# Kernel optimization log

Measured on AMD Instinct MI355X. Metric: run time of the kernel, lower is better.

The kernel has to match this reference:

```python
import jax, jax.numpy as jnp
import numpy as np
from jax import lax

PATCH = 16
TAU = 0.5
EPS = 1e-8  # torch CosineSimilarity default eps


def setup_inputs() -> dict:
    key = jax.random.key(0)
    k1, k2, k3, k4, k5 = jax.random.split(key, 5)
    B, C, HW = 64, 3, 384
    hidden, latent = 768, 1024
    return {
        "x": jax.random.normal(k1, (B, C, HW, HW), dtype=jnp.float32),
        "conv_w": jax.random.normal(k2, (hidden, C, PATCH, PATCH), dtype=jnp.float32) * 0.02,
        "conv_b": jax.random.normal(k3, (hidden,), dtype=jnp.float32) * 0.02,
        "latent1": jax.random.normal(k4, (1, latent, hidden), dtype=jnp.float32),
        "latent2": jax.random.normal(k5, (1, latent, hidden), dtype=jnp.float32),
    }


def _cosine_scores(p, p_norm, lat):
    # p: (B, N, D); lat: (L, D) -> (B, N, L) cosine similarity
    l_norm = jnp.linalg.norm(lat, axis=-1)  # (L,)
    dots = jnp.einsum('bnd,ld->bnl', p, lat)
    denom = jnp.maximum(p_norm[:, :, None] * l_norm[None, None, :], EPS)
    return dots / denom


def reference(x, conv_w, conv_b, latent1, latent2):
    # Patch embedding: Conv2d(kernel=stride=16, padding=0)
    patch = lax.conv_general_dilated(
        x, conv_w, window_strides=(PATCH, PATCH), padding='VALID',
        dimension_numbers=('NCHW', 'OIHW', 'NCHW'))
    patch = patch + conv_b[None, :, None, None]  # (B, D, H', W')
    B, D = patch.shape[0], patch.shape[1]
    p = patch.reshape(B, D, -1).transpose(0, 2, 1)  # (B, N, D)
    p_norm = jnp.linalg.norm(p, axis=-1)  # (B, N)

    far = _cosine_scores(p, p_norm, latent1[0])    # (B, N, L)
    close = _cosine_scores(p, p_norm, latent2[0])  # (B, N, L)

    sum_close = jnp.sum(jnp.exp(close / TAU), axis=(1, 2))  # (B,)
    sum_far = jnp.sum(jnp.exp(far / TAU), axis=(1, 2))      # (B,)
    loss = -jnp.log(sum_close / sum_far)
    return loss.mean()
```

## Files before the change

kernel.cpp:

```cpp
#include <hip/hip_runtime.h>
#include <math.h>

using f32x4  = __attribute__((ext_vector_type(4))) float;
using bf16x8 = __attribute__((ext_vector_type(8))) short;

typedef const __attribute__((address_space(1))) void gas_void;
typedef __attribute__((address_space(3))) void las_void;

__device__ __forceinline__ void gl16(const void* g, void* l) {
    __builtin_amdgcn_global_load_lds((gas_void*)g, (las_void*)l, 16, 0, 0);
}

__device__ __forceinline__ unsigned short f2bf(float f) {
    union { float f; unsigned u; } v; v.f = f;
    unsigned r = v.u + 0x7fffu + ((v.u >> 16) & 1u);
    return (unsigned short)(r >> 16);
}
__device__ __forceinline__ float bf2f(unsigned short u) {
    return __uint_as_float(((unsigned)u) << 16);
}

#define VW0() asm volatile("s_waitcnt vmcnt(0)")
#define BAR() __builtin_amdgcn_s_barrier()

__global__ void pcl_prep_x(const float* __restrict__ x, unsigned short* __restrict__ xp) {
    int t = threadIdx.x;
    int wv = t >> 6, l = t & 63;
    int p = blockIdx.x * 4 + wv;
    int b = p / 576, n = p % 576;
    int ph = n / 24, pw = n % 24;
    const float* base = x + ((size_t)(b * 3)) * 147456 + (ph * 16) * 384 + pw * 16;
    unsigned* dst = (unsigned*)(xp + (size_t)p * 768);
#pragma unroll
    for (int q = 0; q < 6; ++q) {
        int k = q * 128 + l * 2;
        int c = k >> 8, i = (k >> 4) & 15, j = k & 15;
        const float* s = base + (size_t)c * 147456 + i * 384 + j;
        float2 v = *(const float2*)s;
        unsigned lo = f2bf(v.x), hi = f2bf(v.y);
        dst[q * 64 + l] = lo | (hi << 16);
    }
}

__global__ void pcl_prep_wl(const float* __restrict__ w,
                            const float* __restrict__ l1, const float* __restrict__ l2,
                            unsigned short* __restrict__ wsW,
                            unsigned short* __restrict__ wsL) {
    int r = blockIdx.x, t = threadIdx.x;
    if (r < 768) {
        const float* src = w + (size_t)r * 768;
        unsigned short* dst = wsW + (size_t)r * 768;
#pragma unroll
        for (int i = 0; i < 12; ++i) dst[t + 64 * i] = f2bf(src[t + 64 * i]);
    } else {
        int lr = r - 768;
        const float* src = (lr < 1024) ? l1 + (size_t)lr * 768 : l2 + (size_t)(lr - 1024) * 768;
        unsigned short* dst = wsL + (size_t)lr * 768;
        float vals[12];
        float s = 0.f;
#pragma unroll
        for (int i = 0; i < 12; ++i) {
            float f = bf2f(f2bf(src[t + 64 * i]));
            vals[i] = f; s += f * f;
        }
#pragma unroll
        for (int off = 32; off; off >>= 1) s += __shfl_xor(s, off, 64);
        float rn = 1.0f / sqrtf(s);
#pragma unroll
        for (int i = 0; i < 12; ++i) dst[t + 64 * i] = f2bf(vals[i] * rn);
    }
}

#define K1_LDS 81920

__global__ __launch_bounds__(256, 2)
void pcl_k1(const unsigned short* __restrict__ xp,
            const unsigned short* __restrict__ wsW,
            const float* __restrict__ bias,
            unsigned short* __restrict__ pbuf,
            float* __restrict__ rpnp) {
    extern __shared__ char smem[];
    const int t = threadIdx.x, w = t >> 6, l = t & 63;
    const int wg = (blockIdx.x & 7) * 192 + (blockIdx.x >> 3);
    const int mt = wg >> 3, nt = wg & 7;
    const size_t Mb = (size_t)mt * 192;
    const int Nb = nt * 96;
    const int wm = w >> 1, wn = w & 1;
    const int ir = l >> 3, s2 = (l & 7) ^ ir;
    const int lm = l & 15, lg4 = l >> 4;

    char* buf0 = smem;
    char* buf1 = smem + 40960;

    auto stage = [&](int kt, char* buf) {
#pragma unroll
        for (int rr = 0; rr < 6; ++rr) {
            int c2 = w * 6 + rr;
            gl16(xp + (Mb + c2 * 8 + ir) * 768 + kt * 64 + s2 * 8, buf + c2 * 1024);
        }
#pragma unroll
        for (int rr = 0; rr < 3; ++rr) {
            int c2 = w * 3 + rr;
            gl16(wsW + (size_t)(Nb + c2 * 8 + ir) * 768 + kt * 64 + s2 * 8,
                 buf + 24576 + c2 * 1024);
        }
    };

    f32x4 acc[6][3];
#pragma unroll
    for (int m = 0; m < 6; ++m)
#pragma unroll
        for (int nb = 0; nb < 3; ++nb) acc[m][nb] = (f32x4)0.f;

    stage(0, buf0);
    VW0(); BAR();

    bf16x8 areg[3][2], breg[3][2];

#pragma unroll 2
    for (int kt = 0; kt < 12; ++kt) {
        char* cur = (kt & 1) ? buf1 : buf0;
        char* nxt = (kt & 1) ? buf0 : buf1;

        if (kt < 11) stage(kt + 1, nxt);

#pragma unroll
        for (int nb = 0; nb < 3; ++nb)
#pragma unroll
            for (int ks = 0; ks < 2; ++ks) {
                int rb = wn * 48 + nb * 16 + lm, slot = ks * 4 + lg4;
                breg[nb][ks] = *(const bf16x8*)(cur + 24576 + rb * 128 + ((slot ^ (rb & 7)) << 4));
            }
#pragma unroll
        for (int m = 0; m < 3; ++m)
#pragma unroll
            for (int ks = 0; ks < 2; ++ks) {
                int r = wm * 96 + m * 16 + lm, slot = ks * 4 + lg4;
                areg[m][ks] = *(const bf16x8*)(cur + r * 128 + ((slot ^ (r & 7)) << 4));
            }
        __builtin_amdgcn_s_setprio(1);
#pragma unroll
        for (int m = 0; m < 3; ++m)
#pragma unroll
            for (int nb = 0; nb < 3; ++nb)
#pragma unroll
                for (int ks = 0; ks < 2; ++ks)
                    acc[m][nb] = __builtin_amdgcn_mfma_f32_16x16x32_bf16(areg[m][ks], breg[nb][ks], acc[m][nb], 0, 0, 0);
        __builtin_amdgcn_s_setprio(0);

#pragma unroll
        for (int m = 0; m < 3; ++m)
#pragma unroll
            for (int ks = 0; ks < 2; ++ks) {
                int r = wm * 96 + 48 + m * 16 + lm, slot = ks * 4 + lg4;
                areg[m][ks] = *(const bf16x8*)(cur + r * 128 + ((slot ^ (r & 7)) << 4));
            }
        __builtin_amdgcn_s_setprio(1);
#pragma unroll
        for (int m = 0; m < 3; ++m)
#pragma unroll
            for (int nb = 0; nb < 3; ++nb)
#pragma unroll
                for (int ks = 0; ks < 2; ++ks)
                    acc[3 + m][nb] = __builtin_amdgcn_mfma_f32_16x16x32_bf16(areg[m][ks], breg[nb][ks], acc[3 + m][nb], 0, 0, 0);
        __builtin_amdgcn_s_setprio(0);

        VW0();
        BAR();
    }

    float rs[6][4];
#pragma unroll
    for (int m = 0; m < 6; ++m)
#pragma unroll
        for (int j = 0; j < 4; ++j) rs[m][j] = 0.f;
#pragma unroll
    for (int nb = 0; nb < 3; ++nb) {
        int d = Nb + wn * 48 + nb * 16 + lm;
        float bv = bias[d];
#pragma unroll
        for (int m = 0; m < 6; ++m) {
            int mh = m / 3, mi = m % 3;
#pragma unroll
            for (int j = 0; j < 4; ++j) {
                int row = wm * 96 + mh * 48 + mi * 16 + lg4 * 4 + j;
                unsigned short h = f2bf(acc[m][nb][j] + bv);
                pbuf[(Mb + row) * 768 + d] = h;
                float fv = bf2f(h);
                rs[m][j] += fv * fv;
            }
        }
    }
#pragma unroll
    for (int m = 0; m < 6; ++m)
#pragma unroll
        for (int j = 0; j < 4; ++j) {
            rs[m][j] += __shfl_xor(rs[m][j], 1);
            rs[m][j] += __shfl_xor(rs[m][j], 2);
            rs[m][j] += __shfl_xor(rs[m][j], 4);
            rs[m][j] += __shfl_xor(rs[m][j], 8);
        }
    __syncthreads();
    float* nrm = (float*)smem;
    if (lm == 0) {
#pragma unroll
        for (int m = 0; m < 6; ++m) {
            int mh = m / 3, mi = m % 3;
#pragma unroll
            for (int j = 0; j < 4; ++j) {
                int row = wm * 96 + mh * 48 + mi * 16 + lg4 * 4 + j;
                nrm[row * 2 + wn] = rs[m][j];
            }
        }
    }
    __syncthreads();
    if (t < 192) rpnp[(size_t)nt * 36864 + Mb + t] = nrm[t * 2] + nrm[t * 2 + 1];
}

__global__ void pcl_norm(const float* __restrict__ rpnp, float* __restrict__ rpn) {
    int i = blockIdx.x * 256 + threadIdx.x;
    float s = 0.f;
#pragma unroll
    for (int nt = 0; nt < 8; ++nt) s += rpnp[(size_t)nt * 36864 + i];
    rpn[i] = 1.0f / sqrtf(s);
}

#define K2_LDS 81920

__global__ __launch_bounds__(256, 2)
void pcl_k2(const unsigned short* __restrict__ pbuf,
            const unsigned short* __restrict__ wsL,
            const float* __restrict__ rpn,
            double* __restrict__ partials) {
    extern __shared__ char smem[];
    const int t = threadIdx.x, w = t >> 6, l = t & 63;
    const int wg = (blockIdx.x & 7) * 384 + (blockIdx.x >> 3);
    const int mt = wg >> 4, nt = wg & 15;
    const size_t Mb = (size_t)mt * 192;
    const int Nb = nt * 128;
    const int wm = w >> 1, wn = w & 1;
    const int ir = l >> 3, s2 = (l & 7) ^ ir;
    const int lm = l & 15, lg4 = l >> 4;

    char* buf0 = smem;
    char* buf1 = smem + 40960;

    auto stage = [&](int kt, char* buf) {
#pragma unroll
        for (int rr = 0; rr < 6; ++rr) {
            int c2 = w * 6 + rr;
            gl16(pbuf + (Mb + c2 * 8 + ir) * 768 + kt * 64 + s2 * 8, buf + c2 * 1024);
        }
#pragma unroll
        for (int rr = 0; rr < 4; ++rr) {
            int c2 = w * 4 + rr;
            gl16(wsL + (size_t)(Nb + c2 * 8 + ir) * 768 + kt * 64 + s2 * 8,
                 buf + 24576 + c2 * 1024);
        }
    };

    f32x4 acc[6][4];
#pragma unroll
    for (int m = 0; m < 6; ++m)
#pragma unroll
        for (int nb = 0; nb < 4; ++nb) acc[m][nb] = (f32x4)0.f;

    stage(0, buf0);
    VW0(); BAR();

    bf16x8 areg[3][2], breg[4][2];

#pragma unroll 2
    for (int kt = 0; kt < 12; ++kt) {
        char* cur = (kt & 1) ? buf1 : buf0;
        char* nxt = (kt & 1) ? buf0 : buf1;

        if (kt < 11) stage(kt + 1, nxt);

#pragma unroll
        for (int nb = 0; nb < 4; ++nb)
#pragma unroll
            for (int ks = 0; ks < 2; ++ks) {
                int rb = wn * 64 + nb * 16 + lm, slot = ks * 4 + lg4;
                breg[nb][ks] = *(const bf16x8*)(cur + 24576 + rb * 128 + ((slot ^ (rb & 7)) << 4));
            }
#pragma unroll
        for (int m = 0; m < 3; ++m)
#pragma unroll
            for (int ks = 0; ks < 2; ++ks) {
                int r = wm * 96 + m * 16 + lm, slot = ks * 4 + lg4;
                areg[m][ks] = *(const bf16x8*)(cur + r * 128 + ((slot ^ (r & 7)) << 4));
            }
        __builtin_amdgcn_s_setprio(1);
#pragma unroll
        for (int m = 0; m < 3; ++m)
#pragma unroll
            for (int nb = 0; nb < 4; ++nb)
#pragma unroll
                for (int ks = 0; ks < 2; ++ks)
                    acc[m][nb] = __builtin_amdgcn_mfma_f32_16x16x32_bf16(areg[m][ks], breg[nb][ks], acc[m][nb], 0, 0, 0);
        __builtin_amdgcn_s_setprio(0);

#pragma unroll
        for (int m = 0; m < 3; ++m)
#pragma unroll
            for (int ks = 0; ks < 2; ++ks) {
                int r = wm * 96 + 48 + m * 16 + lm, slot = ks * 4 + lg4;
                areg[m][ks] = *(const bf16x8*)(cur + r * 128 + ((slot ^ (r & 7)) << 4));
            }
        __builtin_amdgcn_s_setprio(1);
#pragma unroll
        for (int m = 0; m < 3; ++m)
#pragma unroll
            for (int nb = 0; nb < 4; ++nb)
#pragma unroll
                for (int ks = 0; ks < 2; ++ks)
                    acc[3 + m][nb] = __builtin_amdgcn_mfma_f32_16x16x32_bf16(areg[m][ks], breg[nb][ks], acc[3 + m][nb], 0, 0, 0);
        __builtin_amdgcn_s_setprio(0);

        VW0();
        BAR();
    }

    double ssum = 0.0;
#pragma unroll
    for (int m = 0; m < 6; ++m) {
        int mh = m / 3, mi = m % 3;
        int rl = wm * 96 + mh * 48 + mi * 16;
        float rv[4];
#pragma unroll
        for (int j = 0; j < 4; ++j) rv[j] = rpn[Mb + rl + lg4 * 4 + j];
        float es = 0.f;
#pragma unroll
        for (int nb = 0; nb < 4; ++nb)
#pragma unroll
            for (int j = 0; j < 4; ++j)
                es += __expf(2.0f * acc[m][nb][j] * rv[j]);
        ssum += (double)es;
    }
#pragma unroll
    for (int off = 32; off; off >>= 1) ssum += __shfl_down(ssum, off);
    __syncthreads();
    double* red = (double*)smem;
    if (l == 0) red[w] = ssum;
    __syncthreads();
    if (t == 0) {
        double s = 0.0;
#pragma unroll
        for (int i = 0; i < 4; ++i) s += red[i];
        partials[wg] = s;
    }
}

__global__ void pcl_finish(const double* __restrict__ partials, float* __restrict__ out) {
    int b = threadIdx.x;
    double far = 0.0, close = 0.0;
#pragma unroll
    for (int i = 0; i < 3; ++i) {
        int mt = b * 3 + i;
#pragma unroll
        for (int nTile = 0; nTile < 16; ++nTile) {
            double v = partials[mt * 16 + nTile];
            if (nTile < 8) far += v; else close += v;
        }
    }
    double lb = log(far) - log(close);
#pragma unroll
    for (int off = 32; off; off >>= 1) lb += __shfl_down(lb, off);
    if (b == 0) out[0] = (float)(lb * (1.0 / 64.0));
}

extern "C" void kernel_launch(void* const* d_in, const int* in_sizes, int n_in,
                              void* d_out, int out_size, void* d_ws, size_t ws_size,
                              hipStream_t stream) {
    const float* x    = (const float*)d_in[0];
    const float* w    = (const float*)d_in[1];
    const float* bias = (const float*)d_in[2];
    const float* l1   = (const float*)d_in[3];
    const float* l2   = (const float*)d_in[4];
    float* out = (float*)d_out;

    unsigned short* xp   = (unsigned short*)d_ws;
    unsigned short* pbuf = (unsigned short*)((char*)d_ws + 56623104);
    unsigned short* wsW  = (unsigned short*)((char*)d_ws + 113246208);
    unsigned short* wsL  = (unsigned short*)((char*)d_ws + 114425856);
    float* rpnp          = (float*)((char*)d_ws + 117571584);
    float* rpn           = (float*)((char*)d_ws + 118751232);
    double* partials     = (double*)((char*)d_ws + 118898688);

    (void)hipFuncSetAttribute((const void*)pcl_k1,
                              hipFuncAttributeMaxDynamicSharedMemorySize, K1_LDS);
    (void)hipFuncSetAttribute((const void*)pcl_k2,
                              hipFuncAttributeMaxDynamicSharedMemorySize, K2_LDS);

    pcl_prep_x<<<9216, 256, 0, stream>>>(x, xp);
    pcl_prep_wl<<<2816, 64, 0, stream>>>(w, l1, l2, wsW, wsL);
    pcl_k1<<<1536, 256, K1_LDS, stream>>>(xp, wsW, bias, pbuf, rpnp);
    pcl_norm<<<144, 256, 0, stream>>>(rpnp, rpn);
    pcl_k2<<<3072, 256, K2_LDS, stream>>>(pbuf, wsL, rpn, partials);
    pcl_finish<<<1, 64, 0, stream>>>(partials, out);
}
```

Before: 194.8 us.

## Load A operand directly to registers, stage only B through LDS

In both GEMM kernels the A-tile (patch rows) is no longer staged through LDS. Each wave now loads its own A fragments from global memory straight into double-buffered registers, while only the B tile still goes through the LDS double buffer. The wait before each barrier becomes a partial vmcnt(12), so the next tile's A register loads can stay in flight across the barrier. A sched_barrier pins the order of the issued loads. This cuts LDS traffic and footprint, and it saves the separate LDS reads for A. The cost is much higher VGPR pressure from two 6x2 A register sets, A global loads that are not coalesced, and reliance on an exact vmcnt count.

```diff
diff --git a/kernel.cpp b/kernel.cpp
--- a/kernel.cpp
+++ b/kernel.cpp
@@ -20,8 +20,10 @@
     return __uint_as_float(((unsigned)u) << 16);
 }
 
-#define VW0() asm volatile("s_waitcnt vmcnt(0)")
+#define VWB() asm volatile("s_waitcnt vmcnt(12)" ::: "memory")
+#define VW0() asm volatile("s_waitcnt vmcnt(0)" ::: "memory")
 #define BAR() __builtin_amdgcn_s_barrier()
+#define SCHEDPIN() __builtin_amdgcn_sched_barrier(0)
 
 __global__ void pcl_prep_x(const float* __restrict__ x, unsigned short* __restrict__ xp) {
     int t = threadIdx.x;
@@ -71,7 +73,7 @@
     }
 }
 
-#define K1_LDS 81920
+#define K1_LDS 24576
 
 __global__ __launch_bounds__(256, 2)
 void pcl_k1(const unsigned short* __restrict__ xp,
@@ -90,20 +92,27 @@
     const int lm = l & 15, lg4 = l >> 4;
 
     char* buf0 = smem;
-    char* buf1 = smem + 40960;
-
-    auto stage = [&](int kt, char* buf) {
-#pragma unroll
-        for (int rr = 0; rr < 6; ++rr) {
-            int c2 = w * 6 + rr;
-            gl16(xp + (Mb + c2 * 8 + ir) * 768 + kt * 64 + s2 * 8, buf + c2 * 1024);
-        }
+    char* buf1 = smem + 12288;
+
+    const unsigned short* pA = xp + (Mb + wm * 96 + lm) * 768 + lg4 * 8;
+
+    auto stageB = [&](int kt, char* buf) {
 #pragma unroll
         for (int rr = 0; rr < 3; ++rr) {
             int c2 = w * 3 + rr;
             gl16(wsW + (size_t)(Nb + c2 * 8 + ir) * 768 + kt * 64 + s2 * 8,
-                 buf + 24576 + c2 * 1024);
-        }
+                 buf + c2 * 1024);
+        }
+    };
+    auto loadA = [&](int kt, bf16x8 (&aN)[6][2]) {
+#pragma unroll
+        for (int mh = 0; mh < 2; ++mh)
+#pragma unroll
+            for (int mi = 0; mi < 3; ++mi)
+#pragma unroll
+                for (int ks = 0; ks < 2; ++ks)
+                    aN[mh * 3 + mi][ks] = *(const bf16x8*)
+                        (pA + (size_t)(mh * 48 + mi * 16) * 768 + kt * 64 + ks * 32);
     };
 
     f32x4 acc[6][3];
@@ -112,61 +121,37 @@
 #pragma unroll
         for (int nb = 0; nb < 3; ++nb) acc[m][nb] = (f32x4)0.f;
 
-    stage(0, buf0);
+    bf16x8 aP[6][2], aQ[6][2], breg[3][2];
+
+    loadA(0, aP);
+    stageB(0, buf0);
     VW0(); BAR();
 
-    bf16x8 areg[3][2], breg[3][2];
-
-#pragma unroll 2
-    for (int kt = 0; kt < 12; ++kt) {
-        char* cur = (kt & 1) ? buf1 : buf0;
-        char* nxt = (kt & 1) ? buf0 : buf1;
-
-        if (kt < 11) stage(kt + 1, nxt);
-
+    auto body = [&](int kt, bf16x8 (&aC)[6][2], bf16x8 (&aN)[6][2], char* cur, char* nxt) {
+        if (kt < 11) { stageB(kt + 1, nxt); SCHEDPIN(); loadA(kt + 1, aN); }
 #pragma unroll
         for (int nb = 0; nb < 3; ++nb)
 #pragma unroll
             for (int ks = 0; ks < 2; ++ks) {
                 int rb = wn * 48 + nb * 16 + lm, slot = ks * 4 + lg4;
-                breg[nb][ks] = *(const bf16x8*)(cur + 24576 + rb * 128 + ((slot ^ (rb & 7)) << 4));
-            }
-#pragma unroll
-        for (int m = 0; m < 3; ++m)
-#pragma unroll
-            for (int ks = 0; ks < 2; ++ks) {
-                int r = wm * 96 + m * 16 + lm, slot = ks * 4 + lg4;
-                areg[m][ks] = *(const bf16x8*)(cur + r * 128 + ((slot ^ (r & 7)) << 4));
+                breg[nb][ks] = *(const bf16x8*)(cur + rb * 128 + ((slot ^ (rb & 7)) << 4));
             }
         __builtin_amdgcn_s_setprio(1);
 #pragma unroll
-        for (int m = 0; m < 3; ++m)
+        for (int m = 0; m < 6; ++m)
 #pragma unroll
             for (int nb = 0; nb < 3; ++nb)
 #pragma unroll
                 for (int ks = 0; ks < 2; ++ks)
-                    acc[m][nb] = __builtin_amdgcn_mfma_f32_16x16x32_bf16(areg[m][ks], breg[nb][ks], acc[m][nb], 0, 0, 0);
+                    acc[m][nb] = __builtin_amdgcn_mfma_f32_16x16x32_bf16(aC[m][ks], breg[nb][ks], acc[m][nb], 0, 0, 0);
         __builtin_amdgcn_s_setprio(0);
-
-#pragma unroll
-        for (int m = 0; m < 3; ++m)
-#pragma unroll
-            for (int ks = 0; ks < 2; ++ks) {
-                int r = wm * 96 + 48 + m * 16 + lm, slot = ks * 4 + lg4;
-                areg[m][ks] = *(const bf16x8*)(cur + r * 128 + ((slot ^ (r & 7)) << 4));
-            }
-        __builtin_amdgcn_s_setprio(1);
-#pragma unroll
-        for (int m = 0; m < 3; ++m)
-#pragma unroll
-            for (int nb = 0; nb < 3; ++nb)
-#pragma unroll
-                for (int ks = 0; ks < 2; ++ks)
-                    acc[3 + m][nb] = __builtin_amdgcn_mfma_f32_16x16x32_bf16(areg[m][ks], breg[nb][ks], acc[3 + m][nb], 0, 0, 0);
-        __builtin_amdgcn_s_setprio(0);
-
-        VW0();
+        if (kt < 11) { VWB(); } else { VW0(); }
         BAR();
+    };
+
+    for (int kp = 0; kp < 6; ++kp) {
+        body(2 * kp,     aP, aQ, buf0, buf1);
+        body(2 * kp + 1, aQ, aP, buf1, buf0);
     }
 
     float rs[6][4];
@@ -225,7 +210,7 @@
     rpn[i] = 1.0f / sqrtf(s);
 }
 
-#define K2_LDS 81920
+#define K2_LDS 32768
 
 __global__ __launch_bounds__(256, 2)
 void pcl_k2(const unsigned short* __restrict__ pbuf,
@@ -243,20 +228,27 @@
     const int lm = l & 15, lg4 = l >> 4;
 
     char* buf0 = smem;
-    char* buf1 = smem + 40960;
-
-    auto stage = [&](int kt, char* buf) {
-#pragma unroll
-        for (int rr = 0; rr < 6; ++rr) {
-            int c2 = w * 6 + rr;
-            gl16(pbuf + (Mb + c2 * 8 + ir) * 768 + kt * 64 + s2 * 8, buf + c2 * 1024);
-        }
+    char* buf1 = smem + 16384;
+
+    const unsigned short* pA = pbuf + (Mb + wm * 96 + lm) * 768 + lg4 * 8;
+
+    auto stageB = [&](int kt, char* buf) {
 #pragma unroll
         for (int rr = 0; rr < 4; ++rr) {
             int c2 = w * 4 + rr;
             gl16(wsL + (size_t)(Nb + c2 * 8 + ir) * 768 + kt * 64 + s2 * 8,
-                 buf + 24576 + c2 * 1024);
-        }
+                 buf + c2 * 1024);
+        }
+    };
+    auto loadA = [&](int kt, bf16x8 (&aN)[6][2]) {
+#pragma unroll
+        for (int mh = 0; mh < 2; ++mh)
+#pragma unroll
+            for (int mi = 0; mi < 3; ++mi)
+#pragma unroll
+                for (int ks = 0; ks < 2; ++ks)
+                    aN[mh * 3 + mi][ks] = *(const bf16x8*)
+                        (pA + (size_t)(mh * 48 + mi * 16) * 768 + kt * 64 + ks * 32);
     };
 
     f32x4 acc[6][4];
@@ -265,61 +257,37 @@
 #pragma unroll
         for (int nb = 0; nb < 4; ++nb) acc[m][nb] = (f32x4)0.f;
 
-    stage(0, buf0);
+    bf16x8 aP[6][2], aQ[6][2], breg[4][2];
+
+    loadA(0, aP);
+    stageB(0, buf0);
     VW0(); BAR();
 
-    bf16x8 areg[3][2], breg[4][2];
-
-#pragma unroll 2
-    for (int kt = 0; kt < 12; ++kt) {
-        char* cur = (kt & 1) ? buf1 : buf0;
-        char* nxt = (kt & 1) ? buf0 : buf1;
-
-        if (kt < 11) stage(kt + 1, nxt);
-
+    auto body = [&](int kt, bf16x8 (&aC)[6][2], bf16x8 (&aN)[6][2], char* cur, char* nxt) {
+        if (kt < 11) { stageB(kt + 1, nxt); SCHEDPIN(); loadA(kt + 1, aN); }
 #pragma unroll
         for (int nb = 0; nb < 4; ++nb)
 #pragma unroll
             for (int ks = 0; ks < 2; ++ks) {
                 int rb = wn * 64 + nb * 16 + lm, slot = ks * 4 + lg4;
-                breg[nb][ks] = *(const bf16x8*)(cur + 24576 + rb * 128 + ((slot ^ (rb & 7)) << 4));
-            }
-#pragma unroll
-        for (int m = 0; m < 3; ++m)
-#pragma unroll
-            for (int ks = 0; ks < 2; ++ks) {
-                int r = wm * 96 + m * 16 + lm, slot = ks * 4 + lg4;
-                areg[m][ks] = *(const bf16x8*)(cur + r * 128 + ((slot ^ (r & 7)) << 4));
+                breg[nb][ks] = *(const bf16x8*)(cur + rb * 128 + ((slot ^ (rb & 7)) << 4));
             }
         __builtin_amdgcn_s_setprio(1);
 #pragma unroll
-        for (int m = 0; m < 3; ++m)
+        for (int m = 0; m < 6; ++m)
 #pragma unroll
             for (int nb = 0; nb < 4; ++nb)
 #pragma unroll
                 for (int ks = 0; ks < 2; ++ks)
-                    acc[m][nb] = __builtin_amdgcn_mfma_f32_16x16x32_bf16(areg[m][ks], breg[nb][ks], acc[m][nb], 0, 0, 0);
+                    acc[m][nb] = __builtin_amdgcn_mfma_f32_16x16x32_bf16(aC[m][ks], breg[nb][ks], acc[m][nb], 0, 0, 0);
         __builtin_amdgcn_s_setprio(0);
-
-#pragma unroll
-        for (int m = 0; m < 3; ++m)
-#pragma unroll
-            for (int ks = 0; ks < 2; ++ks) {
-                int r = wm * 96 + 48 + m * 16 + lm, slot = ks * 4 + lg4;
-                areg[m][ks] = *(const bf16x8*)(cur + r * 128 + ((slot ^ (r & 7)) << 4));
-            }
-        __builtin_amdgcn_s_setprio(1);
-#pragma unroll
-        for (int m = 0; m < 3; ++m)
-#pragma unroll
-            for (int nb = 0; nb < 4; ++nb)
-#pragma unroll
-                for (int ks = 0; ks < 2; ++ks)
-                    acc[3 + m][nb] = __builtin_amdgcn_mfma_f32_16x16x32_bf16(areg[m][ks], breg[nb][ks], acc[3 + m][nb], 0, 0, 0);
-        __builtin_amdgcn_s_setprio(0);
-
-        VW0();
+        if (kt < 11) { VWB(); } else { VW0(); }
         BAR();
+    };
+
+    for (int kp = 0; kp < 6; ++kp) {
+        body(2 * kp,     aP, aQ, buf0, buf1);
+        body(2 * kp + 1, aQ, aP, buf1, buf0);
     }
 
     double ssum = 0.0;
```

New measurement: 406.0 us. 108% more time.

## Load GEMM A operand directly from global into registers, shrink LDS to B only

Applied to the files above, without the earlier changes.

The second GEMM kernel now uses 512 threads (8 waves) with each wave owning 48 rows, loading the patch-embedding A operand straight from global memory into registers instead of staging it through LDS. Only the latent B tile is double-buffered in LDS, shrinking shared memory from 80 KB to 32 KB so more blocks fit per CU. A partial vmcnt wait and sched_barrier pins keep the B prefetch in flight. The trade-off is uncoalesced per-lane 16-byte global loads for A with latency exposed in the loop, plus fewer accumulators per wave.

```diff
diff --git a/kernel.cpp b/kernel.cpp
--- a/kernel.cpp
+++ b/kernel.cpp
@@ -20,8 +20,10 @@
     return __uint_as_float(((unsigned)u) << 16);
 }
 
-#define VW0() asm volatile("s_waitcnt vmcnt(0)")
+#define VW2() asm volatile("s_waitcnt vmcnt(2)" ::: "memory")
+#define VW0() asm volatile("s_waitcnt vmcnt(0)" ::: "memory")
 #define BAR() __builtin_amdgcn_s_barrier()
+#define SCHEDPIN() __builtin_amdgcn_sched_barrier(0)
 
 __global__ void pcl_prep_x(const float* __restrict__ x, unsigned short* __restrict__ xp) {
     int t = threadIdx.x;
@@ -225,9 +227,9 @@
     rpn[i] = 1.0f / sqrtf(s);
 }
 
-#define K2_LDS 81920
-
-__global__ __launch_bounds__(256, 2)
+#define K2_LDS 32768
+
+__global__ __launch_bounds__(512, 4)
 void pcl_k2(const unsigned short* __restrict__ pbuf,
             const unsigned short* __restrict__ wsL,
             const float* __restrict__ rpn,
@@ -243,53 +245,51 @@
     const int lm = l & 15, lg4 = l >> 4;
 
     char* buf0 = smem;
-    char* buf1 = smem + 40960;
-
-    auto stage = [&](int kt, char* buf) {
-#pragma unroll
-        for (int rr = 0; rr < 6; ++rr) {
-            int c2 = w * 6 + rr;
-            gl16(pbuf + (Mb + c2 * 8 + ir) * 768 + kt * 64 + s2 * 8, buf + c2 * 1024);
-        }
-#pragma unroll
-        for (int rr = 0; rr < 4; ++rr) {
-            int c2 = w * 4 + rr;
+    char* buf1 = smem + 16384;
+
+    const unsigned short* pA = pbuf + (Mb + wm * 48 + lm) * 768 + lg4 * 8;
+
+    auto stageB = [&](int kt, char* buf) {
+#pragma unroll
+        for (int rr = 0; rr < 2; ++rr) {
+            int c2 = w * 2 + rr;
             gl16(wsL + (size_t)(Nb + c2 * 8 + ir) * 768 + kt * 64 + s2 * 8,
-                 buf + 24576 + c2 * 1024);
+                 buf + c2 * 1024);
         }
     };
 
-    f32x4 acc[6][4];
-#pragma unroll
-    for (int m = 0; m < 6; ++m)
+    f32x4 acc[3][4];
+#pragma unroll
+    for (int m = 0; m < 3; ++m)
 #pragma unroll
         for (int nb = 0; nb < 4; ++nb) acc[m][nb] = (f32x4)0.f;
 
-    stage(0, buf0);
-    VW0(); BAR();
-
-    bf16x8 areg[3][2], breg[4][2];
+    bf16x8 a[3][2], breg[4][2];
+
+    stageB(0, buf0);
 
 #pragma unroll 2
     for (int kt = 0; kt < 12; ++kt) {
         char* cur = (kt & 1) ? buf1 : buf0;
         char* nxt = (kt & 1) ? buf0 : buf1;
 
-        if (kt < 11) stage(kt + 1, nxt);
+        if (kt < 11) stageB(kt + 1, nxt);
+        SCHEDPIN();
+#pragma unroll
+        for (int mi = 0; mi < 3; ++mi)
+#pragma unroll
+            for (int ks = 0; ks < 2; ++ks)
+                a[mi][ks] = *(const bf16x8*)(pA + (size_t)(mi * 16) * 768 + kt * 64 + ks * 32);
+        SCHEDPIN();
+        if (kt < 11) { VW2(); } else { VW0(); }
+        BAR();
 
 #pragma unroll
         for (int nb = 0; nb < 4; ++nb)
 #pragma unroll
             for (int ks = 0; ks < 2; ++ks) {
                 int rb = wn * 64 + nb * 16 + lm, slot = ks * 4 + lg4;
-                breg[nb][ks] = *(const bf16x8*)(cur + 24576 + rb * 128 + ((slot ^ (rb & 7)) << 4));
-            }
-#pragma unroll
-        for (int m = 0; m < 3; ++m)
-#pragma unroll
-            for (int ks = 0; ks < 2; ++ks) {
-                int r = wm * 96 + m * 16 + lm, slot = ks * 4 + lg4;
-                areg[m][ks] = *(const bf16x8*)(cur + r * 128 + ((slot ^ (r & 7)) << 4));
+                breg[nb][ks] = *(const bf16x8*)(cur + rb * 128 + ((slot ^ (rb & 7)) << 4));
             }
         __builtin_amdgcn_s_setprio(1);
 #pragma unroll
@@ -298,35 +298,15 @@
             for (int nb = 0; nb < 4; ++nb)
 #pragma unroll
                 for (int ks = 0; ks < 2; ++ks)
-                    acc[m][nb] = __builtin_amdgcn_mfma_f32_16x16x32_bf16(areg[m][ks], breg[nb][ks], acc[m][nb], 0, 0, 0);
+                    acc[m][nb] = __builtin_amdgcn_mfma_f32_16x16x32_bf16(a[m][ks], breg[nb][ks], acc[m][nb], 0, 0, 0);
         __builtin_amdgcn_s_setprio(0);
-
-#pragma unroll
-        for (int m = 0; m < 3; ++m)
-#pragma unroll
-            for (int ks = 0; ks < 2; ++ks) {
-                int r = wm * 96 + 48 + m * 16 + lm, slot = ks * 4 + lg4;
-                areg[m][ks] = *(const bf16x8*)(cur + r * 128 + ((slot ^ (r & 7)) << 4));
-            }
-        __builtin_amdgcn_s_setprio(1);
-#pragma unroll
-        for (int m = 0; m < 3; ++m)
-#pragma unroll
-            for (int nb = 0; nb < 4; ++nb)
-#pragma unroll
-                for (int ks = 0; ks < 2; ++ks)
-                    acc[3 + m][nb] = __builtin_amdgcn_mfma_f32_16x16x32_bf16(areg[m][ks], breg[nb][ks], acc[3 + m][nb], 0, 0, 0);
-        __builtin_amdgcn_s_setprio(0);
-
-        VW0();
         BAR();
     }
 
     double ssum = 0.0;
 #pragma unroll
-    for (int m = 0; m < 6; ++m) {
-        int mh = m / 3, mi = m % 3;
-        int rl = wm * 96 + mh * 48 + mi * 16;
+    for (int m = 0; m < 3; ++m) {
+        int rl = wm * 48 + m * 16;
         float rv[4];
 #pragma unroll
         for (int j = 0; j < 4; ++j) rv[j] = rpn[Mb + rl + lg4 * 4 + j];
@@ -347,7 +327,7 @@
     if (t == 0) {
         double s = 0.0;
 #pragma unroll
-        for (int i = 0; i < 4; ++i) s += red[i];
+        for (int i = 0; i < 8; ++i) s += red[i];
         partials[wg] = s;
     }
 }
@@ -397,6 +377,6 @@
     pcl_prep_wl<<<2816, 64, 0, stream>>>(w, l1, l2, wsW, wsL);
     pcl_k1<<<1536, 256, K1_LDS, stream>>>(xp, wsW, bias, pbuf, rpnp);
     pcl_norm<<<144, 256, 0, stream>>>(rpnp, rpn);
-    pcl_k2<<<3072, 256, K2_LDS, stream>>>(pbuf, wsL, rpn, partials);
+    pcl_k2<<<3072, 512, K2_LDS, stream>>>(pbuf, wsL, rpn, partials);
     pcl_finish<<<1, 64, 0, stream>>>(partials, out);
 }
```

Measured after the change: 318.6 us. +63.5%, slower.
